# Kernel optimization log

Measured on AMD Instinct MI355X. Metric: run time of the kernel, lower is better.

The kernel has to match this reference:

```python
import jax, jax.numpy as jnp
import numpy as np

DT = 0.02
Z_DIM = 32
U_DIM = 16


def _mlp(x, layers):
    # layers: list of (W, b); SiLU between all but last layer
    n = len(layers)
    for i, (W, b) in enumerate(layers):
        x = x @ W + b
        if i < n - 1:
            x = jax.nn.silu(x)
    return x


def _forward(x, u,
             e_w1, e_b1, e_w2, e_b2, e_w3, e_b3,
             d_w1, d_b1, d_w2, d_b2, d_w3, d_b3, d_w4, d_b4,
             a_w1, a_b1, a_w2, a_b2, a_w3, a_b3,
             b_w1, b_b1, b_w2, b_b2, b_w3, b_b3):
    # encode
    z = _mlp(x, [(e_w1, e_b1), (e_w2, e_b2), (e_w3, e_b3)])          # (B, Z)
    # state-dependent A(x) parameters: pairs (a_i, b_i) per 2x2 block
    aux = _mlp(x, [(a_w1, a_b1), (a_w2, a_b2), (a_w3, a_b3)])        # (B, Z)
    a = aux[:, 0::2]                                                  # (B, Z/2)
    b = aux[:, 1::2]
    f = jnp.exp(a * DT)
    c = jnp.cos(b * DT)
    s = jnp.sin(b * DT)
    # A(x) @ z without materializing block-diagonal: per-pair rotation-scale
    z0 = z[:, 0::2]
    z1 = z[:, 1::2]
    Az = jnp.stack([f * (c * z0 - s * z1), f * (s * z0 + c * z1)], axis=-1).reshape(z.shape)
    # B(x) @ u
    Bmat = _mlp(x, [(b_w1, b_b1), (b_w2, b_b2), (b_w3, b_b3)]).reshape(-1, Z_DIM, U_DIM)
    Bu = jnp.einsum('bzu,bu->bz', Bmat, u)
    # latent Euler step + decode
    z_next = z + DT * (Az + Bu)
    return _mlp(z_next, [(d_w1, d_b1), (d_w2, d_b2), (d_w3, d_b3), (d_w4, d_b4)])


def setup_inputs() -> dict:
    key = jax.random.key(0)
    ks = iter(jax.random.split(key, 32))
    def w(shape, scale=0.02):
        return jax.random.normal(next(ks), shape, jnp.float32) * scale
    B, X, U, Z, H, A = 16384, 64, 16, 32, 1024, 256
    return {
        'x': jax.random.normal(next(ks), (B, X), jnp.float32),
        'u': jax.random.normal(next(ks), (B, U), jnp.float32),
        'e_w1': w((X, H)), 'e_b1': w((H,)),
        'e_w2': w((H, H)), 'e_b2': w((H,)),
        'e_w3': w((H, Z)), 'e_b3': w((Z,)),
        'd_w1': w((Z, H)), 'd_b1': w((H,)),
        'd_w2': w((H, H)), 'd_b2': w((H,)),
        'd_w3': w((H, H)), 'd_b3': w((H,)),
        'd_w4': w((H, X)), 'd_b4': w((X,)),
        'a_w1': w((X, A)), 'a_b1': w((A,)),
        'a_w2': w((A, A)), 'a_b2': w((A,)),
        'a_w3': w((A, Z)), 'a_b3': w((Z,)),
        'b_w1': w((X, A)), 'b_b1': w((A,)),
        'b_w2': w((A, A)), 'b_b2': w((A,)),
        'b_w3': w((A, Z * U)), 'b_b3': w((Z * U,)),
    }


def reference(x, u,
              e_w1, e_b1, e_w2, e_b2, e_w3, e_b3,
              d_w1, d_b1, d_w2, d_b2, d_w3, d_b3, d_w4, d_b4,
              a_w1, a_b1, a_w2, a_b2, a_w3, a_b3,
              b_w1, b_b1, b_w2, b_b2, b_w3, b_b3):
    return _forward(x, u,
                    e_w1, e_b1, e_w2, e_b2, e_w3, e_b3,
                    d_w1, d_b1, d_w2, d_b2, d_w3, d_b3, d_w4, d_b4,
                    a_w1, a_b1, a_w2, a_b2, a_w3, a_b3,
                    b_w1, b_b1, b_w2, b_b2, b_w3, b_b3)
```

## Files before the change

### kernel.cpp

```cpp
#include <hip/hip_runtime.h>
#include <cstdint>
#include <cstddef>

#define B_SZ 16384
#define X_D  64
#define U_D  16
#define Z_D  32
#define H_D  1024
#define A_D  256
#define DT_C 0.02f

typedef _Float16 f16;
typedef f16   f16x8 __attribute__((ext_vector_type(8)));
typedef f16   f16x4 __attribute__((ext_vector_type(4)));
typedef float f32x4 __attribute__((ext_vector_type(4)));

#define AS1 __attribute__((address_space(1)))
#define AS3 __attribute__((address_space(3)))

__device__ __forceinline__ void gld_lds16(const void* g, void* l) {
    __builtin_amdgcn_global_load_lds((AS1 void*)(g), (AS3 void*)(l), 16, 0, 0);
}

struct GArg {
    const f16*  A;
    const f16*  W;
    const float* bias;
    void*       C;
    int lda, ldc, K;
};
struct GSet { GArg g[3]; int yn0, yn1; };

template<int BM,int BN,int BK,int WM,int WN,bool SILU,int OM>
__launch_bounds__(256)
__global__ void gemm_k(GSet p)
{
    static_assert(OM != 1 || BN == 128, "OM1 repack assumes BN=128");
    int yb = blockIdx.y, gi = 0;
    if (yb >= p.yn0) { yb -= p.yn0; gi = 1; if (yb >= p.yn1) { yb -= p.yn1; gi = 2; } }
    const GArg ga = p.g[gi];

    constexpr int SEGROW = BK / 8;
    constexpr int SMASK  = (SEGROW < 8 ? SEGROW : 8) - 1;
    constexpr int WTM = BM / WM, WTN = BN / WN;
    constexpr int RM = WTM / 16, RN = WTN / 16;
    constexpr int ITA = (BM * SEGROW) / 256;
    constexpr int ITB = (BN * SEGROW) / 256;

    constexpr int STAGE_B = (BM + BN) * BK * 2;
    constexpr int CS_B    = (OM == 1) ? BM * BN * 2 : 0;
    constexpr int SMEM_B  = STAGE_B > CS_B ? STAGE_B : CS_B;
    __shared__ __align__(16) char smem[SMEM_B];
    f16* As = (f16*)smem;
    f16* Bs = As + BM * BK;

    const int tid  = threadIdx.x;
    const int lane = tid & 63;
    const int wave = tid >> 6;
    const int wm = wave / WN, wn = wave % WN;
    const int l15 = lane & 15, quad = lane >> 4;

    const size_t arow0 = (size_t)blockIdx.x * BM;
    const size_t brow0 = (size_t)yb * BN;
    const int lda = ga.lda, K = ga.K;

    f32x4 zero = {0.f, 0.f, 0.f, 0.f};
    f32x4 acc[RM][RN];
#pragma unroll
    for (int i = 0; i < RM; ++i)
#pragma unroll
        for (int j = 0; j < RN; ++j) acc[i][j] = zero;

    for (int k0 = 0; k0 < K; k0 += BK) {
#pragma unroll
        for (int it = 0; it < ITA; ++it) {
            int s = it * 256 + tid;
            int row = s / SEGROW, st = s % SEGROW;
            int sg = st ^ (row & SMASK);
            gld_lds16(ga.A + (arow0 + row) * lda + k0 + sg * 8, &As[s * 8]);
        }
#pragma unroll
        for (int it = 0; it < ITB; ++it) {
            int s = it * 256 + tid;
            int row = s / SEGROW, st = s % SEGROW;
            int sg = st ^ (row & SMASK);
            gld_lds16(ga.W + (brow0 + row) * K + k0 + sg * 8, &Bs[s * 8]);
        }
        __syncthreads();

#pragma unroll
        for (int kk = 0; kk < BK; kk += 32) {
            f16x8 af[RM], bf[RN];
#pragma unroll
            for (int i = 0; i < RM; ++i) {
                int row = wm * WTM + i * 16 + l15;
                int st  = ((kk >> 3) + quad) ^ (row & SMASK);
                af[i] = *(const f16x8*)&As[(row * SEGROW + st) * 8];
            }
#pragma unroll
            for (int j = 0; j < RN; ++j) {
                int row = wn * WTN + j * 16 + l15;
                int st  = ((kk >> 3) + quad) ^ (row & SMASK);
                bf[j] = *(const f16x8*)&Bs[(row * SEGROW + st) * 8];
            }
#pragma unroll
            for (int i = 0; i < RM; ++i)
#pragma unroll
                for (int j = 0; j < RN; ++j)
                    acc[i][j] = __builtin_amdgcn_mfma_f32_16x16x32_f16(
                        af[i], bf[j], acc[i][j], 0, 0, 0);
        }
        __syncthreads();
    }

    const int rowbL = wm * WTM;
    const int colbL = wn * WTN;

    if constexpr (OM == 1) {
        f16* Cs = (f16*)smem;
#pragma unroll
        for (int j = 0; j < RN; ++j) {
            int colL = colbL + j * 16 + l15;
            float bv = ga.bias[(int)brow0 + colL];
            int chL = colL >> 3, wi = colL & 7;
#pragma unroll
            for (int i = 0; i < RM; ++i) {
#pragma unroll
                for (int r = 0; r < 4; ++r) {
                    int rowL = rowbL + i * 16 + quad * 4 + r;
                    float v = acc[i][j][r] + bv;
                    if (SILU) v = v / (1.0f + __expf(-v));
                    Cs[rowL * BN + ((chL ^ (rowL & 15)) << 3) + wi] = (f16)v;
                }
            }
        }
        __syncthreads();
        f16* Cout = (f16*)ga.C;
#pragma unroll
        for (int pass = 0; pass < (BM * BN / 8) / 256; ++pass) {
            int s = pass * 256 + tid;
            int rowL = s >> 4;
            int ch = s & 15;
            f16x8 v = *(const f16x8*)&Cs[rowL * BN + ((ch ^ (rowL & 15)) << 3)];
            *(f16x8*)&Cout[(size_t)(arow0 + rowL) * ga.ldc + brow0 + ch * 8] = v;
        }
    } else {
        float* Cout = (float*)ga.C;
#pragma unroll
        for (int j = 0; j < RN; ++j) {
            int col = (int)brow0 + colbL + j * 16 + l15;
            float bv = ga.bias[col];
#pragma unroll
            for (int i = 0; i < RM; ++i) {
#pragma unroll
                for (int r = 0; r < 4; ++r) {
                    int row = (int)arow0 + rowbL + i * 16 + quad * 4 + r;
                    float v = acc[i][j][r] + bv;
                    if (SILU) v = v / (1.0f + __expf(-v));
                    Cout[(size_t)row * ga.ldc + col] = v;
                }
            }
        }
    }
}

__launch_bounds__(256)
__global__ void mid_k(const f16* __restrict__ cc2,
                      const f16* __restrict__ e_w3t, const float* __restrict__ e_b3,
                      const f16* __restrict__ a_w3t, const float* __restrict__ a_b3,
                      const f16* __restrict__ b_w3t, const float* __restrict__ b_b3,
                      const float* __restrict__ u,   f16* __restrict__ znb)
{
    __shared__ __align__(16) f16 As[32 * 64];
    __shared__ __align__(16) f16 Bs[128 * 64];
    __shared__ float zb[32 * 32];
    __shared__ float ab[32 * 32];
    __shared__ float bu[32 * 32];
    __shared__ float ub[32 * 16];

    const int tid  = threadIdx.x;
    const int lane = tid & 63, wave = tid >> 6;
    const int l15 = lane & 15, quad = lane >> 4;
    const int r0 = blockIdx.x * 32;

    ub[tid]       = u[r0 * 16 + tid];
    ub[tid + 256] = u[r0 * 16 + 256 + tid];

#pragma unroll 1
    for (int ph = 0; ph < 2; ++ph) {
        const f16* W    = ph ? a_w3t : e_w3t;
        const float* bs = ph ? a_b3 : e_b3;
        const int K     = ph ? 256 : 1024;
        const int co    = ph ? 1024 : 0;
        float* ob       = ph ? ab : zb;
        f32x4 acc = {0.f, 0.f, 0.f, 0.f};
        for (int k0 = 0; k0 < K; k0 += 64) {
            {
                int row = tid >> 3, sg = (tid & 7) ^ (row & 7);
                gld_lds16(cc2 + (size_t)(r0 + row) * 1536 + co + k0 + sg * 8,
                          &As[tid * 8]);
            }
            {
                int row = tid >> 3, sg = (tid & 7) ^ (row & 7);
                gld_lds16(W + (size_t)row * K + k0 + sg * 8, &Bs[tid * 8]);
            }
            __syncthreads();
#pragma unroll
            for (int kk = 0; kk < 64; kk += 32) {
                int ar = ((wave >> 1) << 4) + l15;
                int ast = ((kk >> 3) + quad) ^ (ar & 7);
                f16x8 af = *(const f16x8*)&As[(ar * 8 + ast) * 8];
                int br = ((wave & 1) << 4) + l15;
                int bst = ((kk >> 3) + quad) ^ (br & 7);
                f16x8 bf = *(const f16x8*)&Bs[(br * 8 + bst) * 8];
                acc = __builtin_amdgcn_mfma_f32_16x16x32_f16(af, bf, acc, 0, 0, 0);
            }
            __syncthreads();
        }
#pragma unroll
        for (int r = 0; r < 4; ++r) {
            int row = ((wave >> 1) << 4) + quad * 4 + r;
            int col = ((wave & 1) << 4) + l15;
            ob[row * 32 + col] = acc[r] + bs[col];
        }
    }

#pragma unroll 1
    for (int ch = 0; ch < 4; ++ch) {
        f32x4 acc[2][2];
#pragma unroll
        for (int i = 0; i < 2; ++i)
#pragma unroll
            for (int j = 0; j < 2; ++j) acc[i][j] = f32x4{0.f, 0.f, 0.f, 0.f};
        for (int k0 = 0; k0 < 256; k0 += 64) {
            {   int row = tid >> 3, sg = (tid & 7) ^ (row & 7);
                gld_lds16(cc2 + (size_t)(r0 + row) * 1536 + 1280 + k0 + sg * 8,
                          &As[tid * 8]);
            }
#pragma unroll
            for (int it = 0; it < 4; ++it) {
                int s = it * 256 + tid;
                int row = s >> 3, sg = (s & 7) ^ (row & 7);
                gld_lds16(b_w3t + (size_t)(ch * 128 + row) * 256 + k0 + sg * 8,
                          &Bs[s * 8]);
            }
            __syncthreads();
#pragma unroll
            for (int kk = 0; kk < 64; kk += 32) {
                f16x8 af[2], bf[2];
#pragma unroll
                for (int i = 0; i < 2; ++i) {
                    int ar = i * 16 + l15;
                    int st = ((kk >> 3) + quad) ^ (ar & 7);
                    af[i] = *(const f16x8*)&As[(ar * 8 + st) * 8];
                }
#pragma unroll
                for (int j = 0; j < 2; ++j) {
                    int br = wave * 32 + j * 16 + l15;
                    int st = ((kk >> 3) + quad) ^ (br & 7);
                    bf[j] = *(const f16x8*)&Bs[(br * 8 + st) * 8];
                }
#pragma unroll
                for (int i = 0; i < 2; ++i)
#pragma unroll
                    for (int j = 0; j < 2; ++j)
                        acc[i][j] = __builtin_amdgcn_mfma_f32_16x16x32_f16(
                            af[i], bf[j], acc[i][j], 0, 0, 0);
            }
            __syncthreads();
        }
#pragma unroll
        for (int j = 0; j < 2; ++j) {
            int colg = ch * 128 + wave * 32 + j * 16 + l15;
            float bv = b_b3[colg];
            int z = colg >> 4;
#pragma unroll
            for (int i = 0; i < 2; ++i) {
#pragma unroll
                for (int r = 0; r < 4; ++r) {
                    int row = i * 16 + quad * 4 + r;
                    float v = (acc[i][j][r] + bv) * ub[row * 16 + l15];
                    v += __shfl_xor(v, 8, 16);
                    v += __shfl_xor(v, 4, 16);
                    v += __shfl_xor(v, 2, 16);
                    v += __shfl_xor(v, 1, 16);
                    if (l15 == 0) bu[row * 32 + z] = v;
                }
            }
        }
    }
    __syncthreads();

#pragma unroll
    for (int t = 0; t < 4; ++t) {
        int idx = t * 256 + tid;
        int row = idx >> 5, z = idx & 31;
        int pb = idx & ~1;
        float a  = ab[pb], b = ab[pb + 1];
        float z0 = zb[pb], z1 = zb[pb + 1];
        float f  = __expf(a * DT_C);
        float c_ = __cosf(b * DT_C);
        float s_ = __sinf(b * DT_C);
        float Az = (z & 1) ? f * (s_ * z0 + c_ * z1) : f * (c_ * z0 - s_ * z1);
        float zc = (z & 1) ? z1 : z0;
        znb[(size_t)(r0 + row) * 32 + z] = (f16)(zc + DT_C * (Az + bu[idx]));
    }
}

struct PrepArgs {
    const float* w[13];
    f16*         wt[13];
    int          K[13];
    int          N[13];
    const float* bsrc[3];
    float*       bias1;
    const float* x;
    f16*         xb;
};

__launch_bounds__(256)
__global__ void prep_k(PrepArgs pa, int ntrans, int ncvt)
{
    int bid = blockIdx.x;
    if (bid < ntrans) {
        int i = 0, t;
        for (;; ++i) {
            t = (pa.K[i] >> 5) * (pa.N[i] >> 5);
            if (bid < t) break;
            bid -= t;
        }
        const int K = pa.K[i], N = pa.N[i];
        const int tn = N >> 5;
        const int k0 = (bid / tn) << 5, n0 = (bid % tn) << 5;
        __shared__ float tbuf[32][33];
        const int tx = threadIdx.x & 31, ty = threadIdx.x >> 5;
        const float* src = pa.w[i];
        f16* dst = pa.wt[i];
#pragma unroll
        for (int r = 0; r < 32; r += 8)
            tbuf[ty + r][tx] = src[(size_t)(k0 + ty + r) * N + n0 + tx];
        __syncthreads();
#pragma unroll
        for (int r = 0; r < 32; r += 8)
            dst[(size_t)(n0 + ty + r) * K + k0 + tx] = (f16)tbuf[tx][ty + r];
    } else if (bid < ntrans + ncvt) {
        int i = ((bid - ntrans) * 256 + threadIdx.x) * 4;
        float4 v = *(const float4*)(pa.x + i);
        f16x4 o = {(f16)v.x, (f16)v.y, (f16)v.z, (f16)v.w};
        *(f16x4*)(pa.xb + i) = o;
    } else {
        int idx = (bid - ntrans - ncvt) * 256 + (int)threadIdx.x;
        float v = (idx < 1024) ? pa.bsrc[0][idx]
                : (idx < 1280) ? pa.bsrc[1][idx - 1024]
                               : pa.bsrc[2][idx - 1280];
        pa.bias1[idx] = v;
    }
}

extern "C" void kernel_launch(void* const* d_in, const int* in_sizes, int n_in,
                              void* d_out, int out_size, void* d_ws, size_t ws_size,
                              hipStream_t stream)
{
    (void)in_sizes; (void)n_in; (void)out_size; (void)ws_size;
    const float* x    = (const float*)d_in[0];
    const float* u    = (const float*)d_in[1];
    const float* e_w1 = (const float*)d_in[2];  const float* e_b1 = (const float*)d_in[3];
    const float* e_w2 = (const float*)d_in[4];  const float* e_b2 = (const float*)d_in[5];
    const float* e_w3 = (const float*)d_in[6];  const float* e_b3 = (const float*)d_in[7];
    const float* d_w1 = (const float*)d_in[8];  const float* d_b1 = (const float*)d_in[9];
    const float* d_w2 = (const float*)d_in[10]; const float* d_b2 = (const float*)d_in[11];
    const float* d_w3 = (const float*)d_in[12]; const float* d_b3 = (const float*)d_in[13];
    const float* d_w4 = (const float*)d_in[14]; const float* d_b4 = (const float*)d_in[15];
    const float* a_w1 = (const float*)d_in[16]; const float* a_b1 = (const float*)d_in[17];
    const float* a_w2 = (const float*)d_in[18]; const float* a_b2 = (const float*)d_in[19];
    const float* a_w3 = (const float*)d_in[20]; const float* a_b3 = (const float*)d_in[21];
    const float* b_w1 = (const float*)d_in[22]; const float* b_b1 = (const float*)d_in[23];
    const float* b_w2 = (const float*)d_in[24]; const float* b_b2 = (const float*)d_in[25];
    const float* b_w3 = (const float*)d_in[26]; const float* b_b3 = (const float*)d_in[27];

    char* p = (char*)d_ws;
    auto alloc = [&](size_t nbytes) -> void* {
        void* r = (void*)p;
        p += (nbytes + 255) & ~(size_t)255;
        return r;
    };
    f16*   xb   = (f16*)  alloc((size_t)B_SZ * X_D * 2);
    f16*   cc1  = (f16*)  alloc((size_t)B_SZ * 1536 * 2);
    f16*   cc2  = (f16*)  alloc((size_t)B_SZ * 1536 * 2);
    f16*   znb  = (f16*)  alloc((size_t)B_SZ * Z_D * 2);
    f16*   h1d  = cc1;
    f16*   h2d  = cc2;
    f16*   h3d  = cc1;
    f16*   W1t   = (f16*)alloc((size_t)1536 * X_D * 2);
    float* bias1 = (float*)alloc(1536 * 4);
    f16* e_w2t = (f16*)alloc((size_t)H_D * H_D * 2);
    f16* e_w3t = (f16*)alloc((size_t)Z_D * H_D * 2);
    f16* d_w1t = (f16*)alloc((size_t)H_D * Z_D * 2);
    f16* d_w2t = (f16*)alloc((size_t)H_D * H_D * 2);
    f16* d_w3t = (f16*)alloc((size_t)H_D * H_D * 2);
    f16* d_w4t = (f16*)alloc((size_t)X_D * H_D * 2);
    f16* a_w2t = (f16*)alloc((size_t)A_D * A_D * 2);
    f16* a_w3t = (f16*)alloc((size_t)Z_D * A_D * 2);
    f16* b_w2t = (f16*)alloc((size_t)A_D * A_D * 2);
    f16* b_w3t = (f16*)alloc((size_t)(Z_D * U_D) * A_D * 2);

    PrepArgs pa;
    const float* ws_[13] = {e_w1, e_w2, e_w3, d_w1, d_w2, d_w3, d_w4,
                            a_w1, a_w2, a_w3, b_w1, b_w2, b_w3};
    f16* wts_[13] = {W1t, e_w2t, e_w3t, d_w1t, d_w2t, d_w3t, d_w4t,
                     W1t + (size_t)1024 * X_D, a_w2t, a_w3t,
                     W1t + (size_t)1280 * X_D, b_w2t, b_w3t};
    int Ks_[13] = {X_D, H_D, H_D, Z_D, H_D, H_D, H_D, X_D, A_D, A_D, X_D, A_D, A_D};
    int Ns_[13] = {H_D, H_D, Z_D, H_D, H_D, H_D, X_D, A_D, A_D, Z_D, A_D, A_D, Z_D*U_D};
    int ntrans = 0;
    for (int i = 0; i < 13; ++i) {
        pa.w[i] = ws_[i]; pa.wt[i] = wts_[i]; pa.K[i] = Ks_[i]; pa.N[i] = Ns_[i];
        ntrans += (Ks_[i] >> 5) * (Ns_[i] >> 5);
    }
    pa.bsrc[0] = e_b1; pa.bsrc[1] = a_b1; pa.bsrc[2] = b_b1;
    pa.bias1 = bias1; pa.x = x; pa.xb = xb;
    const int ncvt = (B_SZ * X_D) / 1024;
    prep_k<<<ntrans + ncvt + 6, 256, 0, stream>>>(pa, ntrans, ncvt);

    auto G = [](const f16* A, const f16* W, const float* bias, void* C,
                int lda, int ldc, int K) {
        GArg g; g.A = A; g.W = W; g.bias = bias; g.C = C;
        g.lda = lda; g.ldc = ldc; g.K = K; return g;
    };
    GSet s;

    s.g[0] = G(xb, W1t, bias1, cc1, X_D, 1536, X_D);
    s.yn0 = 12; s.yn1 = 0;
    gemm_k<128,128,64,2,2,true,1><<<dim3(B_SZ/128, 12), 256, 0, stream>>>(s);

    s.g[0] = G(cc1,        e_w2t, e_b2, cc2,        1536, 1536, H_D);
    s.g[1] = G(cc1 + 1024, a_w2t, a_b2, cc2 + 1024, 1536, 1536, A_D);
    s.g[2] = G(cc1 + 1280, b_w2t, b_b2, cc2 + 1280, 1536, 1536, A_D);
    s.yn0 = 8; s.yn1 = 2;
    gemm_k<128,128,64,2,2,true,1><<<dim3(B_SZ/128, 12), 256, 0, stream>>>(s);

    mid_k<<<B_SZ/32, 256, 0, stream>>>(cc2, e_w3t, e_b3, a_w3t, a_b3,
                                       b_w3t, b_b3, u, znb);

    s.yn0 = 8; s.yn1 = 0;
    s.g[0] = G(znb, d_w1t, d_b1, h1d, Z_D, H_D, Z_D);
    gemm_k<128,128,32,2,2,true,1><<<dim3(B_SZ/128, 8), 256, 0, stream>>>(s);

    s.g[0] = G(h1d, d_w2t, d_b2, h2d, H_D, H_D, H_D);
    gemm_k<128,128,64,2,2,true,1><<<dim3(B_SZ/128, 8), 256, 0, stream>>>(s);

    s.g[0] = G(h2d, d_w3t, d_b3, h3d, H_D, H_D, H_D);
    gemm_k<128,128,64,2,2,true,1><<<dim3(B_SZ/128, 8), 256, 0, stream>>>(s);

    s.g[0] = G(h3d, d_w4t, d_b4, d_out, H_D, X_D, H_D);
    s.yn0 = 1;
    gemm_k<64,64,64,2,2,false,0><<<dim3(B_SZ/64, 1), 256, 0, stream>>>(s);
}
```

Before: 370.9 us.

## Fuse decoder first layer into mid kernel and hoist GEMM load pointers

The latent Euler-step result is now kept in shared memory inside mid_k, which then computes the first decoder layer (K=32) directly with 32x32x16 MFMAs and writes the SiLU output to h1d. This drops the znb buffer round-trip and one GEMM launch. Separately, the GEMM kernel precomputes its global load addresses once and increments them by BK each iteration, removing per-iteration index arithmetic. The fused layer writes scalar f16 values with a 2KB row stride, which may coalesce poorly compared with the tiled GEMM's vectorized stores.

Result: no change. 368.6 us (-0.6%).

```diff
diff --git a/kernel.cpp b/kernel.cpp
--- a/kernel.cpp
+++ b/kernel.cpp
@@ -14,6 +14,7 @@
 typedef f16   f16x8 __attribute__((ext_vector_type(8)));
 typedef f16   f16x4 __attribute__((ext_vector_type(4)));
 typedef float f32x4 __attribute__((ext_vector_type(4)));
+typedef float f32x16 __attribute__((ext_vector_type(16)));
 
 #define AS1 __attribute__((address_space(1)))
 #define AS3 __attribute__((address_space(3)))
@@ -23,10 +24,7 @@
 }
 
 struct GArg {
-    const f16*  A;
-    const f16*  W;
-    const float* bias;
-    void*       C;
+    const f16*  A; const f16* W; const float* bias; void* C;
     int lda, ldc, K;
 };
 struct GSet { GArg g[3]; int yn0, yn1; };
@@ -64,27 +62,37 @@
     const size_t brow0 = (size_t)yb * BN;
     const int lda = ga.lda, K = ga.K;
 
-    f32x4 zero = {0.f, 0.f, 0.f, 0.f};
+    const f16* aptr[ITA];
+    const f16* bptr[ITB];
+#pragma unroll
+    for (int it = 0; it < ITA; ++it) {
+        int s = it * 256 + tid;
+        int row = s / SEGROW, st = s % SEGROW;
+        aptr[it] = ga.A + (arow0 + row) * lda + (st ^ (row & SMASK)) * 8;
+    }
+#pragma unroll
+    for (int it = 0; it < ITB; ++it) {
+        int s = it * 256 + tid;
+        int row = s / SEGROW, st = s % SEGROW;
+        bptr[it] = ga.W + (brow0 + row) * K + (st ^ (row & SMASK)) * 8;
+    }
+
     f32x4 acc[RM][RN];
 #pragma unroll
     for (int i = 0; i < RM; ++i)
 #pragma unroll
-        for (int j = 0; j < RN; ++j) acc[i][j] = zero;
+        for (int j = 0; j < RN; ++j) acc[i][j] = f32x4{0.f, 0.f, 0.f, 0.f};
 
     for (int k0 = 0; k0 < K; k0 += BK) {
 #pragma unroll
         for (int it = 0; it < ITA; ++it) {
-            int s = it * 256 + tid;
-            int row = s / SEGROW, st = s % SEGROW;
-            int sg = st ^ (row & SMASK);
-            gld_lds16(ga.A + (arow0 + row) * lda + k0 + sg * 8, &As[s * 8]);
+            gld_lds16(aptr[it], &As[(it * 256 + tid) * 8]);
+            aptr[it] += BK;
         }
 #pragma unroll
         for (int it = 0; it < ITB; ++it) {
-            int s = it * 256 + tid;
-            int row = s / SEGROW, st = s % SEGROW;
-            int sg = st ^ (row & SMASK);
-            gld_lds16(ga.W + (brow0 + row) * K + k0 + sg * 8, &Bs[s * 8]);
+            gld_lds16(bptr[it], &Bs[(it * 256 + tid) * 8]);
+            bptr[it] += BK;
         }
         __syncthreads();
 
@@ -139,8 +147,7 @@
 #pragma unroll
         for (int pass = 0; pass < (BM * BN / 8) / 256; ++pass) {
             int s = pass * 256 + tid;
-            int rowL = s >> 4;
-            int ch = s & 15;
+            int rowL = s >> 4, ch = s & 15;
             f16x8 v = *(const f16x8*)&Cs[rowL * BN + ((ch ^ (rowL & 15)) << 3)];
             *(f16x8*)&Cout[(size_t)(arow0 + rowL) * ga.ldc + brow0 + ch * 8] = v;
         }
@@ -169,7 +176,8 @@
                       const f16* __restrict__ e_w3t, const float* __restrict__ e_b3,
                       const f16* __restrict__ a_w3t, const float* __restrict__ a_b3,
                       const f16* __restrict__ b_w3t, const float* __restrict__ b_b3,
-                      const float* __restrict__ u,   f16* __restrict__ znb)
+                      const f16* __restrict__ d_w1t, const float* __restrict__ d_b1,
+                      const float* __restrict__ u,   f16* __restrict__ h1d)
 {
     __shared__ __align__(16) f16 As[32 * 64];
     __shared__ __align__(16) f16 Bs[128 * 64];
@@ -177,10 +185,12 @@
     __shared__ float ab[32 * 32];
     __shared__ float bu[32 * 32];
     __shared__ float ub[32 * 16];
+    __shared__ f16   zn2[32 * 36];
 
     const int tid  = threadIdx.x;
     const int lane = tid & 63, wave = tid >> 6;
     const int l15 = lane & 15, quad = lane >> 4;
+    const int l31 = lane & 31, half = lane >> 5;
     const int r0 = blockIdx.x * 32;
 
     ub[tid]       = u[r0 * 16 + tid];
@@ -195,13 +205,11 @@
         float* ob       = ph ? ab : zb;
         f32x4 acc = {0.f, 0.f, 0.f, 0.f};
         for (int k0 = 0; k0 < K; k0 += 64) {
-            {
-                int row = tid >> 3, sg = (tid & 7) ^ (row & 7);
+            {   int row = tid >> 3, sg = (tid & 7) ^ (row & 7);
                 gld_lds16(cc2 + (size_t)(r0 + row) * 1536 + co + k0 + sg * 8,
                           &As[tid * 8]);
             }
-            {
-                int row = tid >> 3, sg = (tid & 7) ^ (row & 7);
+            {   int row = tid >> 3, sg = (tid & 7) ^ (row & 7);
                 gld_lds16(W + (size_t)row * K + k0 + sg * 8, &Bs[tid * 8]);
             }
             __syncthreads();
@@ -303,7 +311,38 @@
         float s_ = __sinf(b * DT_C);
         float Az = (z & 1) ? f * (s_ * z0 + c_ * z1) : f * (c_ * z0 - s_ * z1);
         float zc = (z & 1) ? z1 : z0;
-        znb[(size_t)(r0 + row) * 32 + z] = (f16)(zc + DT_C * (Az + bu[idx]));
+        zn2[row * 36 + z] = (f16)(zc + DT_C * (Az + bu[idx]));
+    }
+    __syncthreads();
+
+#pragma unroll 1
+    for (int nb = 0; nb < 8; ++nb) {
+#pragma unroll
+        for (int it = 0; it < 2; ++it) {
+            int s = it * 256 + tid;
+            int row = s >> 2, sg = (s & 3) ^ (row & 3);
+            gld_lds16(d_w1t + (size_t)(nb * 128 + row) * 32 + sg * 8, &Bs[s * 8]);
+        }
+        __syncthreads();
+        f32x16 a1;
+#pragma unroll
+        for (int r = 0; r < 16; ++r) a1[r] = 0.f;
+        const int nl = wave * 32 + l31;
+#pragma unroll
+        for (int ks = 0; ks < 2; ++ks) {
+            f16x8 af = *(const f16x8*)&zn2[l31 * 36 + ks * 16 + half * 8];
+            f16x8 bf = *(const f16x8*)&Bs[nl * 32 + (((ks * 2 + half) ^ (nl & 3)) << 3)];
+            a1 = __builtin_amdgcn_mfma_f32_32x32x16_f16(af, bf, a1, 0, 0, 0);
+        }
+        float bv = d_b1[nb * 128 + nl];
+#pragma unroll
+        for (int r = 0; r < 16; ++r) {
+            int rowD = (r & 3) + 8 * (r >> 2) + 4 * half;
+            float v = a1[r] + bv;
+            v = v / (1.0f + __expf(-v));
+            h1d[(size_t)(r0 + rowD) * 1024 + nb * 128 + nl] = (f16)v;
+        }
+        __syncthreads();
     }
 }
 
@@ -387,7 +426,6 @@
     f16*   xb   = (f16*)  alloc((size_t)B_SZ * X_D * 2);
     f16*   cc1  = (f16*)  alloc((size_t)B_SZ * 1536 * 2);
     f16*   cc2  = (f16*)  alloc((size_t)B_SZ * 1536 * 2);
-    f16*   znb  = (f16*)  alloc((size_t)B_SZ * Z_D * 2);
     f16*   h1d  = cc1;
     f16*   h2d  = cc2;
     f16*   h3d  = cc1;
@@ -429,7 +467,7 @@
     };
     GSet s;
 
-    s.g[0] = G(xb, W1t, bias1, cc1, X_D, 1536, X_D);
+    s.g[0] = s.g[1] = s.g[2] = G(xb, W1t, bias1, cc1, X_D, 1536, X_D);
     s.yn0 = 12; s.yn1 = 0;
     gemm_k<128,128,64,2,2,true,1><<<dim3(B_SZ/128, 12), 256, 0, stream>>>(s);
 
@@ -440,19 +478,17 @@
     gemm_k<128,128,64,2,2,true,1><<<dim3(B_SZ/128, 12), 256, 0, stream>>>(s);
 
     mid_k<<<B_SZ/32, 256, 0, stream>>>(cc2, e_w3t, e_b3, a_w3t, a_b3,
-                                       b_w3t, b_b3, u, znb);
-
+                                       b_w3t, b_b3, d_w1t, d_b1, u, h1d);
+
+    s.g[0] = s.g[1] = s.g[2] = G(h1d, d_w2t, d_b2, h2d, H_D, H_D, H_D);
     s.yn0 = 8; s.yn1 = 0;
-    s.g[0] = G(znb, d_w1t, d_b1, h1d, Z_D, H_D, Z_D);
-    gemm_k<128,128,32,2,2,true,1><<<dim3(B_SZ/128, 8), 256, 0, stream>>>(s);
-
-    s.g[0] = G(h1d, d_w2t, d_b2, h2d, H_D, H_D, H_D);
     gemm_k<128,128,64,2,2,true,1><<<dim3(B_SZ/128, 8), 256, 0, stream>>>(s);
 
-    s.g[0] = G(h2d, d_w3t, d_b3, h3d, H_D, H_D, H_D);
+    s.g[0] = s.g[1] = s.g[2] = G(h2d, d_w3t, d_b3, h3d, H_D, H_D, H_D);
+    s.yn0 = 8; s.yn1 = 0;
     gemm_k<128,128,64,2,2,true,1><<<dim3(B_SZ/128, 8), 256, 0, stream>>>(s);
 
-    s.g[0] = G(h3d, d_w4t, d_b4, d_out, H_D, X_D, H_D);
-    s.yn0 = 1;
+    s.g[0] = s.g[1] = s.g[2] = G(h3d, d_w4t, d_b4, d_out, H_D, X_D, H_D);
+    s.yn0 = 1; s.yn1 = 0;
     gemm_k<64,64,64,2,2,false,0><<<dim3(B_SZ/64, 1), 256, 0, stream>>>(s);
 }
```
